# Kernel tuning notes

Measured on AMD Instinct MI355X. Metric: run time of the kernel, lower is better.

Reference implementation:

```python
import jax, jax.numpy as jnp
import numpy as np

B, L, D = 2, 2048, 1024
H = 16
HD = D // H            # 64
HALF = HD // 2         # 32
PHASE_SCALE = 1.0
SCALE = HD ** -0.5


def _orthogonal_projection(rng, d, m):
    g = rng.standard_normal((d, m)).astype(np.float32)
    q, r = np.linalg.qr(g)
    s = np.sign(np.diagonal(r))
    s = np.where(s == 0, 1.0, s).astype(np.float32)
    q = q * s[None, :]
    q = q * np.sqrt(d / m)  # preserve_variance=True
    return jnp.asarray(q)


def setup_inputs() -> dict:
    key = jax.random.key(0)
    ks = jax.random.split(key, 6)
    rng = np.random.default_rng(0)
    return {
        "x": jax.random.normal(ks[0], (B, L, D), dtype=jnp.float32),
        "p": jax.random.normal(ks[1], (B, L, D), dtype=jnp.float32),
        "Wqkv": jax.random.normal(ks[2], (D, 3 * D), dtype=jnp.float32) * (D ** -0.5),
        "bqkv": jax.random.normal(ks[3], (3 * D,), dtype=jnp.float32) * 0.02,
        "Wout": jax.random.normal(ks[4], (D, D), dtype=jnp.float32) * (D ** -0.5),
        "bout": jax.random.normal(ks[5], (D,), dtype=jnp.float32) * 0.02,
        "proj": _orthogonal_projection(rng, D, D // 2),
    }


def _rotate_half(t, cos, sin):
    # non-interleaved rotary: split head_dim in halves
    t1, t2 = t[..., :HALF], t[..., HALF:]
    return jnp.concatenate((t1 * cos - t2 * sin, t1 * sin + t2 * cos), axis=-1)


def reference(x, p, Wqkv, bqkv, Wout, bout, proj):
    Bx, Lx = x.shape[0], x.shape[1]
    # QKV projection -> (B, L, 3, H, HD)
    qkv = (x @ Wqkv + bqkv).reshape(Bx, Lx, 3, H, HD)
    q, k, v = qkv[:, :, 0], qkv[:, :, 1], qkv[:, :, 2]
    # collaborative rotary phases from conditioning tokens p
    phases = (p @ proj).reshape(Bx, Lx, H, HALF) * PHASE_SCALE
    cos, sin = jnp.cos(phases), jnp.sin(phases)
    q = _rotate_half(q, cos, sin)
    k = _rotate_half(k, cos, sin)
    # non-causal softmax attention, scale = head_dim^-0.5
    scores = jnp.einsum("blhd,bmhd->bhlm", q, k) * SCALE
    attn = jax.nn.softmax(scores, axis=-1)
    out = jnp.einsum("bhlm,bmhd->blhd", attn, v).reshape(Bx, Lx, D)
    return out @ Wout + bout
```

## Files before the change

kernel.cpp:

```cpp
#include <hip/hip_runtime.h>


typedef __bf16 bf16;
typedef __bf16 bf16x8 __attribute__((ext_vector_type(8)));
typedef __bf16 bf16x4 __attribute__((ext_vector_type(4)));
typedef float f32x4 __attribute__((ext_vector_type(4)));
typedef float f32x16 __attribute__((ext_vector_type(16)));
typedef unsigned int u32;

__device__ __forceinline__ bf16 f2bf(float f) {
  unsigned u = __builtin_bit_cast(unsigned, f);
  u += 0x7FFFu + ((u >> 16) & 1u);
  unsigned short h = (unsigned short)(u >> 16);
  return __builtin_bit_cast(bf16, h);
}

__device__ __forceinline__ void gload_lds16(const bf16* g, bf16* l) {
  __builtin_amdgcn_global_load_lds((const __attribute__((address_space(1))) u32*)(const void*)g,
                                   (__attribute__((address_space(3))) u32*)(void*)l, 16, 0, 0);
}

__device__ __forceinline__ u32 cvtpk_bf16(float lo, float hi) {
  u32 r;
  asm("v_cvt_pk_bf16_f32 %0, %1, %2" : "=v"(r) : "v"(lo), "v"(hi));
  return r;
}
__device__ __forceinline__ void perm32swap(u32& a, u32& b) {
  asm("v_permlane32_swap_b32 %0, %1" : "+v"(a), "+v"(b));
}

#if __has_builtin(__builtin_amdgcn_exp2f)
#define EXP2(x) __builtin_amdgcn_exp2f(x)
#else
#define EXP2(x) exp2f(x)
#endif

#define QSCALE 0.18033688f

__device__ __forceinline__ void xcd_remap(int& bx, int& by) {
  const int nx = gridDim.x;
  const int nwg = nx * gridDim.y;
  const int lin = blockIdx.y * nx + blockIdx.x;
  const int chunk = nwg >> 3;
  const int nid = (lin & 7) * chunk + (lin >> 3);
  bx = nid % nx;
  by = nid / nx;
}

__global__ __launch_bounds__(256) void k_prep(const float* __restrict__ x, bf16* __restrict__ xb,
                                              const float* __restrict__ p, bf16* __restrict__ pb,
                                              const float* __restrict__ W1, bf16* __restrict__ O1,
                                              const float* __restrict__ W2, bf16* __restrict__ O2,
                                              const float* __restrict__ W3, bf16* __restrict__ O3) {
  const int gb = blockIdx.x;
  if (gb < 8192) {
    int i = gb * 256 + threadIdx.x;
    const float* in = x; bf16* out = xb;
    if (i >= 1048576) { in = p; out = pb; i -= 1048576; }
    const float4 v = ((const float4*)in)[i];
    bf16x4 o;
    o[0] = f2bf(v.x); o[1] = f2bf(v.y); o[2] = f2bf(v.z); o[3] = f2bf(v.w);
    *(bf16x4*)(out + (size_t)i * 4) = o;
    return;
  }
  __shared__ float t[64][65];
  const int lin = gb - 8192;
  int bx = lin % 72;
  const int by = lin / 72;
  const float* in; bf16* out; int C;
  if (bx < 48)      { in = W1; out = O1; C = 3072; }
  else if (bx < 56) { in = W2; out = O2; C = 512;  bx -= 48; }
  else              { in = W3; out = O3; C = 1024; bx -= 56; }
  const int R = 1024;
  const int c0 = bx * 64, r0 = by * 64;
  for (int e = threadIdx.x; e < 4096; e += 256) {
    int r = e >> 6, c = e & 63;
    t[r][c] = in[(size_t)(r0 + r) * C + c0 + c];
  }
  __syncthreads();
  for (int e = threadIdx.x; e < 4096; e += 256) {
    int c = e >> 6, r = e & 63;
    out[(size_t)(c0 + c) * R + r0 + r] = f2bf(t[r][c]);
  }
}

__global__ __launch_bounds__(512, 2) void k_gemm128x8(const bf16* __restrict__ A,
                                                      const bf16* __restrict__ Bt,
                                                      const float* __restrict__ bias,
                                                      float* __restrict__ C,
                                                      int M, int N, int K) {
  __shared__ bf16 sA0[8192], sA1[8192];
  __shared__ bf16 sB0[8192], sB1[8192];
  const int tid = threadIdx.x;
  const int lane = tid & 63, w = tid >> 6;
  const int lrow = lane & 15, lgrp = lane >> 4;
  const int wm = (w >> 2) * 64, wn = (w & 3) * 32;
  int bx, by;
  xcd_remap(bx, by);
  const int m0 = bx * 128, n0 = by * 128;
  const int rsub = lane >> 3, slot = lane & 7;
  const int swz8 = (slot ^ rsub) * 8;
  const int r7 = lrow & 7;
  const int nkt = K >> 6;

  const bf16* Ab = A  + (size_t)m0 * K;
  const bf16* Bb = Bt + (size_t)n0 * K;

  f32x4 acc[4][2] = {};

#pragma unroll
  for (int c = 0; c < 2; ++c) {
    gload_lds16(Ab + (size_t)(c * 64 + w * 8 + rsub) * K + swz8, sA0 + c * 4096 + w * 512);
    gload_lds16(Bb + (size_t)(c * 64 + w * 8 + rsub) * K + swz8, sB0 + c * 4096 + w * 512);
  }
  __syncthreads();

  for (int kt = 0; kt < nkt; ++kt) {
    const bf16* pA = (kt & 1) ? sA1 : sA0;
    const bf16* pB = (kt & 1) ? sB1 : sB0;
    bf16* nA = (kt & 1) ? sA0 : sA1;
    bf16* nB = (kt & 1) ? sB0 : sB1;
    const size_t knext = (size_t)(kt + 1) * 64;
    const bool more = (kt < nkt - 1);

#pragma unroll
    for (int kk = 0; kk < 2; ++kk) {
      bf16x8 af[4], bfr[2];
#pragma unroll
      for (int mi = 0; mi < 4; ++mi)
        af[mi] = *(const bf16x8*)&pA[(wm + mi * 16 + lrow) * 64 + ((kk * 4 + lgrp) ^ r7) * 8];
#pragma unroll
      for (int ni = 0; ni < 2; ++ni)
        bfr[ni] = *(const bf16x8*)&pB[(wn + ni * 16 + lrow) * 64 + ((kk * 4 + lgrp) ^ r7) * 8];
      if (more) {
        const bf16* src = kk ? Bb : Ab;
        bf16* dst = kk ? nB : nA;
#pragma unroll
        for (int c = 0; c < 2; ++c)
          gload_lds16(src + (size_t)(c * 64 + w * 8 + rsub) * K + knext + swz8, dst + c * 4096 + w * 512);
      }
      __builtin_amdgcn_s_setprio(1);
#pragma unroll
      for (int mi = 0; mi < 4; ++mi)
#pragma unroll
        for (int ni = 0; ni < 2; ++ni)
          acc[mi][ni] = __builtin_amdgcn_mfma_f32_16x16x32_bf16(af[mi], bfr[ni], acc[mi][ni], 0, 0, 0);
      __builtin_amdgcn_s_setprio(0);
    }
    __syncthreads();
  }

#pragma unroll
  for (int mi = 0; mi < 4; ++mi)
#pragma unroll
    for (int ni = 0; ni < 2; ++ni) {
      const int col = n0 + wn + ni * 16 + lrow;
      const float bv = bias ? bias[col] : 0.f;
#pragma unroll
      for (int j = 0; j < 4; ++j) {
        const int row = m0 + wm + mi * 16 + lgrp * 4 + j;
        C[(size_t)row * N + col] = acc[mi][ni][j] + bv;
      }
    }
}

__global__ __launch_bounds__(256, 3) void k_gemm64(const bf16* __restrict__ A,
                                                   const bf16* __restrict__ Bt,
                                                   const float* __restrict__ bias,
                                                   float* __restrict__ C,
                                                   int M, int N, int K) {
  __shared__ bf16 sA0[4096], sA1[4096];
  __shared__ bf16 sB0[8192], sB1[8192];
  const int tid = threadIdx.x;
  const int lane = tid & 63, w = tid >> 6;
  const int lrow = lane & 15, lgrp = lane >> 4;
  const int wn = w * 32;
  int bx, by;
  xcd_remap(bx, by);
  const int m0 = bx * 64, n0 = by * 128;
  const int rsub = tid >> 3;
  const int swz8 = ((tid & 7) ^ (rsub & 7)) * 8;
  const int r7 = lrow & 7;
  const int nkt = K >> 6;

  const bf16* Ab = A  + (size_t)m0 * K;
  const bf16* Bb = Bt + (size_t)n0 * K;

  f32x4 acc[4][2] = {};

#pragma unroll
  for (int c = 0; c < 2; ++c)
    gload_lds16(Ab + (size_t)(c * 32 + rsub) * K + swz8, sA0 + c * 2048 + (tid >> 6) * 512 + (tid & 63) / 64  + ((tid & 63) >> 3) * 0 + (tid - (tid >> 6) * 64) * 0 + w * 512);
  __syncthreads();
#pragma unroll
  for (int c = 0; c < 2; ++c)
    gload_lds16(Ab + (size_t)(c * 32 + rsub) * K + swz8, sA0 + c * 2048 + w * 512);
#pragma unroll
  for (int c = 0; c < 4; ++c)
    gload_lds16(Bb + (size_t)(c * 32 + rsub) * K + swz8, sB0 + c * 2048 + w * 512);
  __syncthreads();

  for (int kt = 0; kt < nkt; ++kt) {
    const bf16* pA = (kt & 1) ? sA1 : sA0;
    const bf16* pB = (kt & 1) ? sB1 : sB0;
    bf16* nA = (kt & 1) ? sA0 : sA1;
    bf16* nB = (kt & 1) ? sB0 : sB1;
    const size_t knext = (size_t)(kt + 1) * 64;
    const bool more = (kt < nkt - 1);

#pragma unroll
    for (int kk = 0; kk < 2; ++kk) {
      bf16x8 af[4], bfr[2];
#pragma unroll
      for (int mi = 0; mi < 4; ++mi)
        af[mi] = *(const bf16x8*)&pA[(mi * 16 + lrow) * 64 + ((kk * 4 + lgrp) ^ r7) * 8];
#pragma unroll
      for (int ni = 0; ni < 2; ++ni)
        bfr[ni] = *(const bf16x8*)&pB[(wn + ni * 16 + lrow) * 64 + ((kk * 4 + lgrp) ^ r7) * 8];
      if (more) {
        if (kk == 0) {
#pragma unroll
          for (int c = 0; c < 2; ++c)
            gload_lds16(Ab + (size_t)(c * 32 + rsub) * K + knext + swz8, nA + c * 2048 + w * 512);
        } else {
#pragma unroll
          for (int c = 0; c < 4; ++c)
            gload_lds16(Bb + (size_t)(c * 32 + rsub) * K + knext + swz8, nB + c * 2048 + w * 512);
        }
      }
      __builtin_amdgcn_s_setprio(1);
#pragma unroll
      for (int mi = 0; mi < 4; ++mi)
#pragma unroll
        for (int ni = 0; ni < 2; ++ni)
          acc[mi][ni] = __builtin_amdgcn_mfma_f32_16x16x32_bf16(af[mi], bfr[ni], acc[mi][ni], 0, 0, 0);
      __builtin_amdgcn_s_setprio(0);
    }
    __syncthreads();
  }

#pragma unroll
  for (int mi = 0; mi < 4; ++mi)
#pragma unroll
    for (int ni = 0; ni < 2; ++ni) {
      const int col = n0 + wn + ni * 16 + lrow;
      const float bv = bias ? bias[col] : 0.f;
#pragma unroll
      for (int j = 0; j < 4; ++j) {
        const int row = m0 + mi * 16 + lgrp * 4 + j;
        C[(size_t)row * N + col] = acc[mi][ni][j] + bv;
      }
    }
}

__global__ __launch_bounds__(512, 2) void k_gemm_qkv256(const bf16* __restrict__ A,
                                                        const bf16* __restrict__ Bt,
                                                        const float* __restrict__ bqkv,
                                                        const float* __restrict__ phases,
                                                        bf16* __restrict__ qb,
                                                        bf16* __restrict__ kb,
                                                        bf16* __restrict__ vb) {
  __shared__ bf16 sA0[16384], sA1[16384];
  __shared__ bf16 sB0[16384], sB1[16384];
  const int tid = threadIdx.x;
  const int lane = tid & 63, w = tid >> 6;
  const int lrow = lane & 15, lgrp = lane >> 4;
  const int wm = (w >> 2) * 128;
  const int wn = (w & 3) * 64;
  const int m0 = blockIdx.x * 256, n0 = blockIdx.y * 256;
  const int K = 1024;

  const int srow = tid >> 3;
  const int swz8 = (((tid & 7) ^ (srow & 7))) * 8;
  const int r7 = lrow & 7;

  const bf16* Ab = A  + (size_t)m0 * K;
  const bf16* Bb = Bt + (size_t)n0 * K;

  f32x4 acc[8][4] = {};

#pragma unroll
  for (int g = 0; g < 4; ++g) {
    gload_lds16(Ab + (size_t)(g * 64 + srow) * K + swz8, sA0 + g * 4096 + w * 512);
    gload_lds16(Bb + (size_t)(g * 64 + srow) * K + swz8, sB0 + g * 4096 + w * 512);
  }
  __syncthreads();

  for (int kt = 0; kt < 16; ++kt) {
    const bf16* pA = (kt & 1) ? sA1 : sA0;
    const bf16* pB = (kt & 1) ? sB1 : sB0;
    bf16* nA = (kt & 1) ? sA0 : sA1;
    bf16* nB = (kt & 1) ? sB0 : sB1;
    const size_t knext = (size_t)(kt + 1) * 64;

    bf16x8 bfr[4][2];
#pragma unroll
    for (int ni = 0; ni < 4; ++ni)
#pragma unroll
      for (int kk = 0; kk < 2; ++kk)
        bfr[ni][kk] = *(const bf16x8*)&pB[(wn + ni * 16 + lrow) * 64 + ((kk * 4 + lgrp) ^ r7) * 8];

#pragma unroll
    for (int q = 0; q < 4; ++q) {
      if (kt < 15) {
        gload_lds16(Ab + (size_t)(q * 64 + srow) * K + knext + swz8, nA + q * 4096 + w * 512);
        gload_lds16(Bb + (size_t)(q * 64 + srow) * K + knext + swz8, nB + q * 4096 + w * 512);
      }
      bf16x8 af[2][2];
#pragma unroll
      for (int m2 = 0; m2 < 2; ++m2)
#pragma unroll
        for (int kk = 0; kk < 2; ++kk)
          af[m2][kk] = *(const bf16x8*)&pA[(wm + (q * 2 + m2) * 16 + lrow) * 64 + ((kk * 4 + lgrp) ^ r7) * 8];
      __builtin_amdgcn_s_setprio(1);
#pragma unroll
      for (int m2 = 0; m2 < 2; ++m2)
#pragma unroll
        for (int ni = 0; ni < 4; ++ni)
#pragma unroll
          for (int kk = 0; kk < 2; ++kk)
            acc[q * 2 + m2][ni] =
                __builtin_amdgcn_mfma_f32_16x16x32_bf16(af[m2][kk], bfr[ni][kk], acc[q * 2 + m2][ni], 0, 0, 0);
      __builtin_amdgcn_s_setprio(0);
    }
    __syncthreads();
  }

  const int nw = n0 + wn;
  const int sec = nw >> 10;
  const int hh = (nw & 1023) >> 6;
  const float b0 = bqkv[nw + lrow];
  const float b1 = bqkv[nw + 16 + lrow];
  const float b2 = bqkv[nw + 32 + lrow];
  const float b3 = bqkv[nw + 48 + lrow];

  if (sec == 2) {
#pragma unroll
    for (int mi = 0; mi < 8; ++mi) {
      const int row0 = m0 + wm + mi * 16 + lgrp * 4;
      const int b = row0 >> 11, l0 = row0 & 2047;
#pragma unroll
      for (int ni = 0; ni < 4; ++ni) {
        const int d = ni * 16 + lrow;
        const float bv = (ni == 0) ? b0 : (ni == 1) ? b1 : (ni == 2) ? b2 : b3;
        bf16x4 pv;
#pragma unroll
        for (int j = 0; j < 4; ++j) pv[j] = f2bf(acc[mi][ni][j] + bv);
        *(bf16x4*)&vb[(((size_t)(b * 16 + hh)) * 64 + d) * 2048 + l0] = pv;
      }
    }
  } else {
    bf16* qk = sec ? kb : qb;
    const float qs = sec ? 1.0f : QSCALE;
#pragma unroll
    for (int mi = 0; mi < 8; ++mi) {
#pragma unroll
      for (int j = 0; j < 4; ++j) {
        const int row = m0 + wm + mi * 16 + lgrp * 4 + j;
        const int b = row >> 11, l = row & 2047;
        const float ph1 = phases[(size_t)row * 512 + hh * 32 + lrow];
        const float ph2 = phases[(size_t)row * 512 + hh * 32 + 16 + lrow];
        float s1, c1, s2, c2;
        __sincosf(ph1, &s1, &c1);
        __sincosf(ph2, &s2, &c2);
        const float t0 = acc[mi][0][j] + b0;
        const float t1 = acc[mi][1][j] + b1;
        const float t2 = acc[mi][2][j] + b2;
        const float t3 = acc[mi][3][j] + b3;
        bf16* base = qk + (((size_t)(b * 16 + hh)) * 2048 + l) * 64;
        base[lrow]      = f2bf((t0 * c1 - t2 * s1) * qs);
        base[16 + lrow] = f2bf((t1 * c2 - t3 * s2) * qs);
        base[32 + lrow] = f2bf((t0 * s1 + t2 * c1) * qs);
        base[48 + lrow] = f2bf((t1 * s2 + t3 * c2) * qs);
      }
    }
  }
}

__global__ __launch_bounds__(256, 4) void k_flash_attn5(const bf16* __restrict__ qb,
                                                        const bf16* __restrict__ kb,
                                                        const bf16* __restrict__ vb,
                                                        bf16* __restrict__ attnout) {
  const int tid = threadIdx.x, lane = tid & 63, w = tid >> 6;
  const int ql = lane & 31, hi = lane >> 5;
  const int tsel = w >> 1;
  const int qh = w & 1;
  const int fid = blockIdx.x;
  const int nid = (fid & 7) * 128 + (fid >> 3);
  const int qblk = nid & 31, h = (nid >> 5) & 15, b = nid >> 9;
  const size_t bh = (size_t)b * 16 + h;
  const bf16* Kp = kb + bh * 2048 * 64;
  const bf16* Vp = vb + bh * 64 * 2048;

  __shared__ __align__(16) char smem[32768];
  bf16* sK = (bf16*)smem;
  bf16* sV = (bf16*)(smem + 16384);

  const bf16* Qp = qb + (bh * 2048 + (size_t)qblk * 64 + qh * 32 + ql) * 64;
  bf16x8 qf[4];
#pragma unroll
  for (int c = 0; c < 4; ++c) qf[c] = *(const bf16x8*)(Qp + c * 16 + hi * 8);

  const int srow = tid >> 3;
  const int swz = (tid & 7) ^ (srow & 7);

  f32x16 o0 = {}, o1 = {};
  float lsum = 0.f;

#define STAGE(BUF, KV0)                                                                       \
  do {                                                                                        \
    gload_lds16(Kp + (size_t)((KV0) + srow) * 64 + swz * 8,        sK + (BUF) * 4096 + w * 512); \
    gload_lds16(Kp + (size_t)((KV0) + srow + 32) * 64 + swz * 8,   sK + (BUF) * 4096 + 2048 + w * 512); \
    gload_lds16(Vp + (size_t)srow * 2048 + (KV0) + swz * 8,        sV + (BUF) * 4096 + w * 512); \
    gload_lds16(Vp + (size_t)(srow + 32) * 2048 + (KV0) + swz * 8, sV + (BUF) * 4096 + 2048 + w * 512); \
  } while (0)

  STAGE(0, 0);
  __syncthreads();

  for (int t = 0; t < 32; ++t) {
    const int cur = t & 1;
    if (t < 31) STAGE(cur ^ 1, (t + 1) * 64);

    const bf16* sKc = sK + cur * 4096;
    const bf16* sVc = sV + cur * 4096;

    f32x16 st0 = {};
#pragma unroll
    for (int c = 0; c < 4; ++c) {
      const int j = (c * 2 + hi) ^ (ql & 7);
      bf16x8 kf = *(const bf16x8*)&sKc[(tsel * 32 + ql) * 64 + j * 8];
      __builtin_amdgcn_s_setprio(1);
      st0 = __builtin_amdgcn_mfma_f32_32x32x16_bf16(kf, qf[c], st0, 0, 0, 0);
      __builtin_amdgcn_s_setprio(0);
    }

#pragma unroll
    for (int j2 = 0; j2 < 16; ++j2) {
      float pv = EXP2(st0[j2]);
      st0[j2] = pv; lsum += pv;
    }

#pragma unroll
    for (int fs = 0; fs < 2; ++fs) {
      u32 a0 = cvtpk_bf16(st0[fs * 8 + 0], st0[fs * 8 + 1]);
      u32 a1 = cvtpk_bf16(st0[fs * 8 + 2], st0[fs * 8 + 3]);
      u32 a2 = cvtpk_bf16(st0[fs * 8 + 4], st0[fs * 8 + 5]);
      u32 a3 = cvtpk_bf16(st0[fs * 8 + 6], st0[fs * 8 + 7]);
      perm32swap(a0, a2);
      perm32swap(a1, a3);
      union { u32 u[4]; bf16x8 v; } cu;
      cu.u[0] = a0; cu.u[1] = a1; cu.u[2] = a2; cu.u[3] = a3;
      const int j = (tsel * 4 + fs * 2 + hi) ^ (ql & 7);
      bf16x8 vf0 = *(const bf16x8*)&sVc[ql * 64 + j * 8];
      bf16x8 vf1 = *(const bf16x8*)&sVc[(32 + ql) * 64 + j * 8];
      __builtin_amdgcn_s_setprio(1);
      o0 = __builtin_amdgcn_mfma_f32_32x32x16_bf16(vf0, cu.v, o0, 0, 0, 0);
      o1 = __builtin_amdgcn_mfma_f32_32x32x16_bf16(vf1, cu.v, o1, 0, 0, 0);
      __builtin_amdgcn_s_setprio(0);
    }
    __syncthreads();
  }

  float* cb = (float*)smem;
  if (w >= 2) {
    const int idx = ((w - 2) * 64 + lane) * 34;
#pragma unroll
    for (int i = 0; i < 16; ++i) cb[idx + i] = o0[i];
#pragma unroll
    for (int i = 0; i < 16; ++i) cb[idx + 16 + i] = o1[i];
    cb[idx + 32] = lsum;
  }
  __syncthreads();
  if (w < 2) {
    const int idx = (w * 64 + lane) * 34;
#pragma unroll
    for (int i = 0; i < 16; ++i) o0[i] += cb[idx + i];
#pragma unroll
    for (int i = 0; i < 16; ++i) o1[i] += cb[idx + 16 + i];
    lsum += cb[idx + 32];
    lsum += __shfl_xor(lsum, 32);

    const float inv = 1.f / lsum;
    const int qrow = qblk * 64 + qh * 32 + ql;
    bf16* outp = attnout + ((size_t)b * 2048 + qrow) * 1024 + h * 64;
#pragma unroll
    for (int j2 = 0; j2 < 4; ++j2) {
      bf16x4 ov;
#pragma unroll
      for (int jj = 0; jj < 4; ++jj) ov[jj] = f2bf(o0[j2 * 4 + jj] * inv);
      *(bf16x4*)(outp + j2 * 8 + hi * 4) = ov;
#pragma unroll
      for (int jj = 0; jj < 4; ++jj) ov[jj] = f2bf(o1[j2 * 4 + jj] * inv);
      *(bf16x4*)(outp + 32 + j2 * 8 + hi * 4) = ov;
    }
  }
#undef STAGE
}

extern "C" void kernel_launch(void* const* d_in, const int* in_sizes, int n_in,
                              void* d_out, int out_size, void* d_ws, size_t ws_size,
                              hipStream_t stream) {
  (void)in_sizes; (void)n_in; (void)out_size; (void)ws_size;
  const float* x    = (const float*)d_in[0];
  const float* p    = (const float*)d_in[1];
  const float* Wqkv = (const float*)d_in[2];
  const float* bqkv = (const float*)d_in[3];
  const float* Wout = (const float*)d_in[4];
  const float* bout = (const float*)d_in[5];
  const float* proj = (const float*)d_in[6];
  float* out = (float*)d_out;

  char* ws = (char*)d_ws;
  size_t off = 0;
  bf16* xb     = (bf16*)(ws + off); off += (size_t)4096 * 1024 * 2;
  bf16* pb     = (bf16*)(ws + off); off += (size_t)4096 * 1024 * 2;
  bf16* WqkvT  = (bf16*)(ws + off); off += (size_t)3072 * 1024 * 2;
  bf16* projT  = (bf16*)(ws + off); off += (size_t)512  * 1024 * 2;
  bf16* WoutT  = (bf16*)(ws + off); off += (size_t)1024 * 1024 * 2;
  float* phases= (float*)(ws + off); off += (size_t)4096 * 512 * 4;
  bf16* qb     = (bf16*)(ws + off); off += (size_t)4096 * 1024 * 2;
  bf16* kb     = (bf16*)(ws + off); off += (size_t)4096 * 1024 * 2;
  bf16* vb     = (bf16*)(ws + off); off += (size_t)4096 * 1024 * 2;
  bf16* attnb  = (bf16*)(ws + off); off += (size_t)4096 * 1024 * 2;

  k_prep<<<9344, 256, 0, stream>>>(x, xb, p, pb, Wqkv, WqkvT, proj, projT, Wout, WoutT);

  k_gemm64<<<dim3(64, 4), 256, 0, stream>>>(pb, projT, nullptr, phases, 4096, 512, 1024);
  k_gemm_qkv256<<<dim3(16, 12), 512, 0, stream>>>(xb, WqkvT, bqkv, phases, qb, kb, vb);

  k_flash_attn5<<<1024, 256, 0, stream>>>(qb, kb, vb, attnb);

  k_gemm128x8<<<dim3(32, 8), 512, 0, stream>>>(attnb, WoutT, bout, out, 4096, 1024, 1024);
}
```

Before: 132.5 us.

## Software-pipeline flash attention: overlap previous tile's PV MFMAs with current QK

```diff
diff --git a/kernel.cpp b/kernel.cpp
--- a/kernel.cpp
+++ b/kernel.cpp
@@ -190,10 +190,6 @@
 
 #pragma unroll
   for (int c = 0; c < 2; ++c)
-    gload_lds16(Ab + (size_t)(c * 32 + rsub) * K + swz8, sA0 + c * 2048 + (tid >> 6) * 512 + (tid & 63) / 64  + ((tid & 63) >> 3) * 0 + (tid - (tid >> 6) * 64) * 0 + w * 512);
-  __syncthreads();
-#pragma unroll
-  for (int c = 0; c < 2; ++c)
     gload_lds16(Ab + (size_t)(c * 32 + rsub) * K + swz8, sA0 + c * 2048 + w * 512);
 #pragma unroll
   for (int c = 0; c < 4; ++c)
@@ -377,7 +373,7 @@
   }
 }
 
-__global__ __launch_bounds__(256, 4) void k_flash_attn5(const bf16* __restrict__ qb,
+__global__ __launch_bounds__(256, 4) void k_flash_attn8(const bf16* __restrict__ qb,
                                                         const bf16* __restrict__ kb,
                                                         const bf16* __restrict__ vb,
                                                         bf16* __restrict__ attnout) {
@@ -403,9 +399,13 @@
 
   const int srow = tid >> 3;
   const int swz = (tid & 7) ^ (srow & 7);
+  const int jv0 = (tsel * 4 + 0 + hi) ^ (ql & 7);
+  const int jv1 = (tsel * 4 + 2 + hi) ^ (ql & 7);
 
   f32x16 o0 = {}, o1 = {};
   float lsum = 0.f;
+  u32 pcu[8];
+  bf16x8 vfr[4];
 
 #define STAGE(BUF, KV0)                                                                       \
   do {                                                                                        \
@@ -415,16 +415,48 @@
     gload_lds16(Vp + (size_t)(srow + 32) * 2048 + (KV0) + swz * 8, sV + (BUF) * 4096 + 2048 + w * 512); \
   } while (0)
 
+#define SM_PACK(CUR)                                                                \
+  do {                                                                              \
+    const bf16* sVc = sV + (CUR) * 4096;                                            \
+    _Pragma("unroll")                                                               \
+    for (int j2 = 0; j2 < 16; ++j2) {                                               \
+      float pv = EXP2(st0[j2]);                                                     \
+      st0[j2] = pv; lsum += pv;                                                     \
+    }                                                                               \
+    {                                                                               \
+      u32 a0 = cvtpk_bf16(st0[0], st0[1]),  a1 = cvtpk_bf16(st0[2], st0[3]);        \
+      u32 a2 = cvtpk_bf16(st0[4], st0[5]),  a3 = cvtpk_bf16(st0[6], st0[7]);        \
+      perm32swap(a0, a2); perm32swap(a1, a3);                                       \
+      pcu[0] = a0; pcu[1] = a1; pcu[2] = a2; pcu[3] = a3;                           \
+      u32 b0 = cvtpk_bf16(st0[8], st0[9]),  b1 = cvtpk_bf16(st0[10], st0[11]);      \
+      u32 b2 = cvtpk_bf16(st0[12], st0[13]), b3 = cvtpk_bf16(st0[14], st0[15]);     \
+      perm32swap(b0, b2); perm32swap(b1, b3);                                       \
+      pcu[4] = b0; pcu[5] = b1; pcu[6] = b2; pcu[7] = b3;                           \
+    }                                                                               \
+    vfr[0] = *(const bf16x8*)&sVc[ql * 64 + jv0 * 8];                               \
+    vfr[1] = *(const bf16x8*)&sVc[(32 + ql) * 64 + jv0 * 8];                        \
+    vfr[2] = *(const bf16x8*)&sVc[ql * 64 + jv1 * 8];                               \
+    vfr[3] = *(const bf16x8*)&sVc[(32 + ql) * 64 + jv1 * 8];                        \
+  } while (0)
+
+#define PV_PREV()                                                                   \
+  do {                                                                              \
+    union { u32 u[4]; bf16x8 v; } cA, cB;                                           \
+    cA.u[0] = pcu[0]; cA.u[1] = pcu[1]; cA.u[2] = pcu[2]; cA.u[3] = pcu[3];         \
+    cB.u[0] = pcu[4]; cB.u[1] = pcu[5]; cB.u[2] = pcu[6]; cB.u[3] = pcu[7];         \
+    __builtin_amdgcn_s_setprio(1);                                                  \
+    o0 = __builtin_amdgcn_mfma_f32_32x32x16_bf16(vfr[0], cA.v, o0, 0, 0, 0);        \
+    o1 = __builtin_amdgcn_mfma_f32_32x32x16_bf16(vfr[1], cA.v, o1, 0, 0, 0);        \
+    o0 = __builtin_amdgcn_mfma_f32_32x32x16_bf16(vfr[2], cB.v, o0, 0, 0, 0);        \
+    o1 = __builtin_amdgcn_mfma_f32_32x32x16_bf16(vfr[3], cB.v, o1, 0, 0, 0);        \
+    __builtin_amdgcn_s_setprio(0);                                                  \
+  } while (0)
+
   STAGE(0, 0);
   __syncthreads();
 
-  for (int t = 0; t < 32; ++t) {
-    const int cur = t & 1;
-    if (t < 31) STAGE(cur ^ 1, (t + 1) * 64);
-
-    const bf16* sKc = sK + cur * 4096;
-    const bf16* sVc = sV + cur * 4096;
-
+  {
+    const bf16* sKc = sK;
     f32x16 st0 = {};
 #pragma unroll
     for (int c = 0; c < 4; ++c) {
@@ -434,33 +466,31 @@
       st0 = __builtin_amdgcn_mfma_f32_32x32x16_bf16(kf, qf[c], st0, 0, 0, 0);
       __builtin_amdgcn_s_setprio(0);
     }
-
-#pragma unroll
-    for (int j2 = 0; j2 < 16; ++j2) {
-      float pv = EXP2(st0[j2]);
-      st0[j2] = pv; lsum += pv;
-    }
-
-#pragma unroll
-    for (int fs = 0; fs < 2; ++fs) {
-      u32 a0 = cvtpk_bf16(st0[fs * 8 + 0], st0[fs * 8 + 1]);
-      u32 a1 = cvtpk_bf16(st0[fs * 8 + 2], st0[fs * 8 + 3]);
-      u32 a2 = cvtpk_bf16(st0[fs * 8 + 4], st0[fs * 8 + 5]);
-      u32 a3 = cvtpk_bf16(st0[fs * 8 + 6], st0[fs * 8 + 7]);
-      perm32swap(a0, a2);
-      perm32swap(a1, a3);
-      union { u32 u[4]; bf16x8 v; } cu;
-      cu.u[0] = a0; cu.u[1] = a1; cu.u[2] = a2; cu.u[3] = a3;
-      const int j = (tsel * 4 + fs * 2 + hi) ^ (ql & 7);
-      bf16x8 vf0 = *(const bf16x8*)&sVc[ql * 64 + j * 8];
-      bf16x8 vf1 = *(const bf16x8*)&sVc[(32 + ql) * 64 + j * 8];
+    STAGE(1, 64);
+    SM_PACK(0);
+    __syncthreads();
+  }
+
+  for (int t = 1; t < 32; ++t) {
+    const int cur = t & 1;
+    const bf16* sKc = sK + cur * 4096;
+
+    f32x16 st0 = {};
+#pragma unroll
+    for (int c = 0; c < 4; ++c) {
+      const int j = (c * 2 + hi) ^ (ql & 7);
+      bf16x8 kf = *(const bf16x8*)&sKc[(tsel * 32 + ql) * 64 + j * 8];
       __builtin_amdgcn_s_setprio(1);
-      o0 = __builtin_amdgcn_mfma_f32_32x32x16_bf16(vf0, cu.v, o0, 0, 0, 0);
-      o1 = __builtin_amdgcn_mfma_f32_32x32x16_bf16(vf1, cu.v, o1, 0, 0, 0);
+      st0 = __builtin_amdgcn_mfma_f32_32x32x16_bf16(kf, qf[c], st0, 0, 0, 0);
       __builtin_amdgcn_s_setprio(0);
     }
+    PV_PREV();
+    if (t < 31) STAGE(cur ^ 1, (t + 1) * 64);
+    SM_PACK(cur);
     __syncthreads();
   }
+
+  PV_PREV();
 
   float* cb = (float*)smem;
   if (w >= 2) {
@@ -496,6 +526,8 @@
     }
   }
 #undef STAGE
+#undef SM_PACK
+#undef PV_PREV
 }
 
 extern "C" void kernel_launch(void* const* d_in, const int* in_sizes, int n_in,
@@ -529,7 +561,7 @@
   k_gemm64<<<dim3(64, 4), 256, 0, stream>>>(pb, projT, nullptr, phases, 4096, 512, 1024);
   k_gemm_qkv256<<<dim3(16, 12), 512, 0, stream>>>(xb, WqkvT, bqkv, phases, qb, kb, vb);
 
-  k_flash_attn5<<<1024, 256, 0, stream>>>(qb, kb, vb, attnb);
+  k_flash_attn8<<<1024, 256, 0, stream>>>(qb, kb, vb, attnb);
 
   k_gemm128x8<<<dim3(32, 8), 512, 0, stream>>>(attnb, WoutT, bout, out, 4096, 1024, 1024);
 }
```

Result: no change. 132.3 us (-0.1%).
